# Performance work log

Measured on AMD Instinct MI355X. Metric: run time of the kernel, lower is better.

Reference implementation:

```python
import jax, jax.numpy as jnp
import numpy as np

WS = 7        # window_size
SHIFT = 3     # shift_size
HEADS = 6
DIM = 192
HIDDEN = DIM * 6  # mlp_ratio=6
EPS = 1e-5


def _rel_pos_index(ws):
    # static relative-position index, (ws*ws, ws*ws) int
    coords = np.stack(np.meshgrid(np.arange(ws), np.arange(ws), indexing='ij')).reshape(2, -1)
    rel = coords[:, :, None] - coords[:, None, :]            # (2, N, N)
    rel = rel.transpose(1, 2, 0)                             # (N, N, 2)
    rel[:, :, 0] += ws - 1
    rel[:, :, 1] += ws - 1
    rel[:, :, 0] *= 2 * ws - 1
    return rel.sum(-1)


def _layernorm(t, g, b):
    m = t.mean(-1, keepdims=True)
    v = jnp.mean((t - m) ** 2, axis=-1, keepdims=True)
    return (t - m) * jax.lax.rsqrt(v + EPS) * g + b


def setup_inputs() -> dict:
    key = jax.random.key(0)
    ks = jax.random.split(key, 8)
    B, H, W = 16, 56, 56
    x = jax.random.normal(ks[0], (B, H * W, DIM), dtype=jnp.float32)
    p = lambda k, s: (jax.random.normal(k, s, dtype=jnp.float32) * 0.02)
    return {
        'x': x, 'H': H, 'W': W,
        'ln1_g': jnp.ones((DIM,), jnp.float32), 'ln1_b': jnp.zeros((DIM,), jnp.float32),
        'qkv_w': p(ks[1], (3 * DIM, DIM)), 'qkv_b': jnp.zeros((3 * DIM,), jnp.float32),
        'rpb': p(ks[2], ((2 * WS - 1) ** 2, HEADS)),
        'proj_w': p(ks[3], (DIM, DIM)), 'proj_b': jnp.zeros((DIM,), jnp.float32),
        'ln2_g': jnp.ones((DIM,), jnp.float32), 'ln2_b': jnp.zeros((DIM,), jnp.float32),
        'fc1_w': p(ks[4], (HIDDEN, DIM)), 'fc1_b': jnp.zeros((HIDDEN,), jnp.float32),
        'fc2_w': p(ks[5], (DIM, HIDDEN)), 'fc2_b': jnp.zeros((DIM,), jnp.float32),
    }


def reference(x, H, W, ln1_g, ln1_b, qkv_w, qkv_b, rpb, proj_w, proj_b,
              ln2_g, ln2_b, fc1_w, fc1_b, fc2_w, fc2_b):
    B, L, C = x.shape
    hd = C // HEADS
    shortcut = x
    h = _layernorm(x, ln1_g, ln1_b).reshape(B, H, W, C)
    pad_r = (WS - W % WS) % WS
    pad_b = (WS - H % WS) % WS
    h = jnp.pad(h, ((0, 0), (0, pad_b), (0, pad_r), (0, 0)))
    Hp, Wp = H + pad_b, W + pad_r
    if SHIFT > 0:
        h = jnp.roll(h, (-SHIFT, -SHIFT), axis=(1, 2))
    # window partition -> (nW*B, WS*WS, C)
    h = h.reshape(B, Hp // WS, WS, Wp // WS, WS, C).transpose(0, 1, 3, 2, 4, 5)
    h = h.reshape(-1, WS * WS, C)
    nB, N, _ = h.shape
    qkv = (h @ qkv_w.T + qkv_b).reshape(nB, N, 3, HEADS, hd).transpose(2, 0, 3, 1, 4)
    q, k, v = qkv[0], qkv[1], qkv[2]       # (nB, heads, N, hd)
    scale = hd ** -0.5
    attn = jnp.einsum('bhnd,bhmd->bhnm', q * scale, k)
    idx = _rel_pos_index(WS)
    bias = rpb[idx.reshape(-1)].reshape(N, N, HEADS).transpose(2, 0, 1)  # (heads, N, N)
    attn = jax.nn.softmax(attn + bias[None], axis=-1)
    out = jnp.einsum('bhnm,bhmd->bhnd', attn, v).transpose(0, 2, 1, 3).reshape(nB, N, C)
    out = out @ proj_w.T + proj_b
    # window reverse -> (B, Hp, Wp, C)
    out = out.reshape(B, Hp // WS, Wp // WS, WS, WS, C).transpose(0, 1, 3, 2, 4, 5)
    out = out.reshape(B, Hp, Wp, C)
    if SHIFT > 0:
        out = jnp.roll(out, (SHIFT, SHIFT), axis=(1, 2))
    out = out[:, :H, :W, :].reshape(B, H * W, C)
    x = shortcut + out
    h2 = _layernorm(x, ln2_g, ln2_b)
    h2 = jax.nn.gelu(h2 @ fc1_w.T + fc1_b, approximate=False)
    return x + (h2 @ fc2_w.T + fc2_b)
```

## Files before the change

### kernel.cpp

```cpp
#include <hip/hip_runtime.h>

typedef unsigned short u16;
typedef __bf16 bf16x8 __attribute__((ext_vector_type(8)));
typedef __bf16 bf16x2_t __attribute__((ext_vector_type(2)));
typedef float f32x4 __attribute__((ext_vector_type(4)));

#define AS1 __attribute__((address_space(1)))
#define AS3 __attribute__((address_space(3)))

__device__ __forceinline__ void gld16(const void* g, void* l) {
  __builtin_amdgcn_global_load_lds((const AS1 void*)g, (AS3 void*)l, 16, 0, 0);
}

__device__ __forceinline__ u16 f2bf(float f) {
  union { float f; unsigned int u; } v; v.f = f;
  unsigned int u = v.u;
  u += 0x7fffu + ((u >> 16) & 1u);
  return (u16)(u >> 16);
}
__device__ __forceinline__ float bf2f(u16 h) {
  union { unsigned int u; float f; } v; v.u = ((unsigned int)h) << 16; return v.f;
}
__device__ __forceinline__ unsigned int pk2(float a, float b) {
#if __has_builtin(__builtin_amdgcn_cvt_pk_bf16_f32)
  union { bf16x2_t v; unsigned int u; } c;
  c.v = __builtin_amdgcn_cvt_pk_bf16_f32(a, b);
  return c.u;
#else
  return (unsigned int)f2bf(a) | ((unsigned int)f2bf(b) << 16);
#endif
}
__device__ __forceinline__ float gelu_f(float v) {
  float u = v * (1.5957691216f + 0.0713548163f * v * v);
  return v * __builtin_amdgcn_rcpf(1.0f + __expf(-u));
}

__global__ __launch_bounds__(256) void cast_weights(
    const float* __restrict__ w0, const float* __restrict__ w1,
    const float* __restrict__ w2, const float* __restrict__ w3,
    u16* __restrict__ o0, u16* __restrict__ o1,
    u16* __restrict__ o2, u16* __restrict__ o3) {
  int i = blockIdx.x * 256 + threadIdx.x;
  if (i < 110592) o0[i] = f2bf(w0[i]);
  if (i < 36864) {
    int n = i / 192, kp = i - n * 192;
    int h = kp >> 5, dp = kp & 31;
    int d = (dp & 1) ? ((dp >> 1) + 16) : (dp >> 1);
    o1[i] = f2bf(w1[n * 192 + h * 32 + d]);
  }
  if (i < 221184) o2[i] = f2bf(w2[i]);
  if (i < 221184) o3[i] = f2bf(w3[i]);
}

__global__ __launch_bounds__(256) void build_btab(
    const float* __restrict__ rpb, float* __restrict__ btab) {
  int id = blockIdx.x * 256 + threadIdx.x;
  int head = id >> 12;
  int m = (id >> 6) & 63;
  int r = id & 63;
  float v;
  if (m >= 49) v = -1e30f;
  else if (r >= 49) v = 0.0f;
  else {
    int mi = m / 7, mj = m - mi * 7;
    int ri = r / 7, rj = r - ri * 7;
    v = rpb[((ri - mi + 6) * 13 + (rj - mj + 6)) * 6 + head];
  }
  btab[id] = v;
}

__global__ __launch_bounds__(256) void ln_kernel(
    const float* __restrict__ x, const float* __restrict__ g,
    const float* __restrict__ b, u16* __restrict__ out) {
  int row = blockIdx.x * 4 + (threadIdx.x >> 6);
  int lane = threadIdx.x & 63;
  const float* xr = x + (long)row * 192;
  float e0 = xr[lane], e1 = xr[lane + 64], e2 = xr[lane + 128];
  float s = e0 + e1 + e2;
  #pragma unroll
  for (int o = 1; o < 64; o <<= 1) s += __shfl_xor(s, o);
  float mean = s * (1.0f / 192.0f);
  float d0 = e0 - mean, d1 = e1 - mean, d2 = e2 - mean;
  float q = d0 * d0 + d1 * d1 + d2 * d2;
  #pragma unroll
  for (int o = 1; o < 64; o <<= 1) q += __shfl_xor(q, o);
  float rstd = rsqrtf(q * (1.0f / 192.0f) + 1e-5f);
  u16* orow = out + (long)row * 192;
  orow[lane]       = f2bf(d0 * rstd * g[lane]       + b[lane]);
  orow[lane + 64]  = f2bf(d1 * rstd * g[lane + 64]  + b[lane + 64]);
  orow[lane + 128] = f2bf(d2 * rstd * g[lane + 128] + b[lane + 128]);
}

template<int MODE>
__global__ __launch_bounds__(256, 3) void wsgemm_kernel(
    const u16* __restrict__ A, const u16* __restrict__ W,
    const float* __restrict__ bias, const float* __restrict__ resid,
    void* __restrict__ out, int N) {
  __shared__ u16 wlds[36 * 512];
  const int tid = threadIdx.x;
  const int wave = tid >> 6, lane = tid & 63;
  const int quad = lane >> 4, l15 = lane & 15;
  const int bn = blockIdx.y * 96;
  const long bm = (long)blockIdx.x * 128 + wave * 32;

  bf16x8 af[2][6];
  #pragma unroll
  for (int mt = 0; mt < 2; mt++)
    #pragma unroll
    for (int kc = 0; kc < 6; kc++)
      af[mt][kc] = *(const bf16x8*)&A[(bm + mt * 16 + l15) * 192 + kc * 32 + quad * 8];

  #pragma unroll
  for (int i = 0; i < 9; i++) {
    int t = wave + i * 4;
    int kc = t / 6, nt = t - kc * 6;
    gld16(W + (long)(bn + nt * 16 + l15) * 192 + kc * 32 + quad * 8,
          &wlds[t * 512]);
  }

  float bi[6];
  #pragma unroll
  for (int nt = 0; nt < 6; nt++) bi[nt] = bias[bn + nt * 16 + l15];

  __syncthreads();

  f32x4 acc[2][6] = {};
  #pragma unroll
  for (int kc = 0; kc < 6; kc++) {
    #pragma unroll
    for (int nt = 0; nt < 6; nt++) {
      bf16x8 wf = *(const bf16x8*)&wlds[(kc * 6 + nt) * 512 + lane * 8];
      acc[0][nt] = __builtin_amdgcn_mfma_f32_16x16x32_bf16(af[0][kc], wf, acc[0][nt], 0, 0, 0);
      acc[1][nt] = __builtin_amdgcn_mfma_f32_16x16x32_bf16(af[1][kc], wf, acc[1][nt], 0, 0, 0);
    }
  }

  #pragma unroll
  for (int mt = 0; mt < 2; mt++) {
    #pragma unroll
    for (int nt = 0; nt < 6; nt++) {
      const long col = bn + nt * 16 + l15;
      #pragma unroll
      for (int j = 0; j < 4; j++) {
        const long row = bm + mt * 16 + quad * 4 + j;
        const long idx = row * (long)N + col;
        float v = acc[mt][nt][j] + bi[nt];
        if (MODE == 2) {
          ((float*)out)[idx] = v + resid[idx];
        } else {
          if (MODE == 1) v = gelu_f(v);
          ((u16*)out)[idx] = f2bf(v);
        }
      }
    }
  }
}

template<int MODE>
__global__ __launch_bounds__(256, 3) void gemm_kernel(
    const u16* __restrict__ A, const u16* __restrict__ W,
    const float* __restrict__ bias, const float* __restrict__ resid,
    void* __restrict__ out, int N, int K) {
  constexpr int TT = 20;
  constexpr int BUF = TT * 512;
  __shared__ u16 lds[2 * BUF];
  float* ct = (float*)lds;
  const int tid = threadIdx.x;
  const int wave = tid >> 6, lane = tid & 63;
  const int wm = wave >> 1, wn = wave & 1;
  const int quad = lane >> 4, l15 = lane & 15;
  const long bm = (long)blockIdx.x * 128;
  const int bn = blockIdx.y * 192;
  const int NC = K >> 5;

  const u16* sp[5];
  int sd[5];
  #pragma unroll
  for (int i = 0; i < 5; i++) {
    int t = wave + i * 4;
    sp[i] = (t < 8) ? (A + (bm + t * 16 + l15) * (long)K + quad * 8)
                    : (W + (long)(bn + (t - 8) * 16 + l15) * K + quad * 8);
    sd[i] = t * 512;
  }
  auto stage = [&](u16* dst) {
    #pragma unroll
    for (int i = 0; i < 5; i++) { gld16(sp[i], dst + sd[i]); sp[i] += 32; }
  };

  stage(lds);
  __syncthreads();

  f32x4 acc[4][6] = {};
  for (int c = 0; c < NC; c++) {
    const int cur = c & 1;
    if (c + 1 < NC) stage(&lds[(cur ^ 1) * BUF]);
    const u16* buf = lds + cur * BUF;
    bf16x8 af[4];
    #pragma unroll
    for (int mt = 0; mt < 4; mt++)
      af[mt] = *(const bf16x8*)&buf[(wm * 4 + mt) * 512 + lane * 8];
    #pragma unroll
    for (int nt = 0; nt < 6; nt++) {
      bf16x8 bfr = *(const bf16x8*)&buf[(8 + wn * 6 + nt) * 512 + lane * 8];
      #pragma unroll
      for (int mt = 0; mt < 4; mt++)
        acc[mt][nt] = __builtin_amdgcn_mfma_f32_16x16x32_bf16(af[mt], bfr, acc[mt][nt], 0, 0, 0);
    }
    __syncthreads();
  }

  const int frow = tid >> 2, seg = tid & 3;
  #pragma unroll
  for (int h = 0; h < 2; h++) {
    #pragma unroll
    for (int g = 0; g < 2; g++) {
      if (wm == h && wn == g) {
        #pragma unroll
        for (int nt = 0; nt < 6; nt++) {
          int col = nt * 16 + l15;
          float bi = bias[bn + g * 96 + col];
          #pragma unroll
          for (int mt = 0; mt < 4; mt++) {
            int row0 = mt * 16 + quad * 4;
            #pragma unroll
            for (int j = 0; j < 4; j++)
              ct[(row0 + j) * 100 + col] = acc[mt][nt][j] + bi;
          }
        }
      }
      __syncthreads();
      const float* cp = &ct[frow * 100 + seg * 4];
      long gbase = (bm + h * 64 + frow) * (long)N + bn + g * 96 + seg * 4;
      #pragma unroll
      for (int k = 0; k < 6; k++) {
        float4 v = *(const float4*)(cp + k * 16);
        long idx = gbase + k * 16;
        if (MODE == 2) {
          const float4 rv = *(const float4*)(resid + idx);
          v.x += rv.x; v.y += rv.y; v.z += rv.z; v.w += rv.w;
          *(float4*)((float*)out + idx) = v;
        } else {
          if (MODE == 1) {
            v.x = gelu_f(v.x); v.y = gelu_f(v.y); v.z = gelu_f(v.z); v.w = gelu_f(v.w);
          }
          uint2 pk;
          pk.x = pk2(v.x, v.y);
          pk.y = pk2(v.z, v.w);
          *(uint2*)((u16*)out + idx) = pk;
        }
      }
      if (!(h == 1 && g == 1)) __syncthreads();
    }
  }
}

__global__ __launch_bounds__(256) void attn_kernel(
    const u16* __restrict__ qkv, const float* __restrict__ btab,
    u16* __restrict__ attn) {
  __shared__ u16 lds[4 * 7040];
  __shared__ float sbias[64 * 65];
  int tid = threadIdx.x;
  int wave = tid >> 6, lane = tid & 63;
  int quad = lane >> 4, l15 = lane & 15;
  int head = blockIdx.x % 6;
  int grp = blockIdx.x / 6;
  int win = grp * 4 + wave;
  int b = win >> 6, wy = (win >> 3) & 7, wx = win & 7;
  u16* lp = lds + wave * 7040;
  u16* lvt = lp + 4608;
  float* rsum = (float*)(lp + 6912);

  {
    const float* bsrc = btab + head * 4096;
    #pragma unroll
    for (int i = 0; i < 4; i++) {
      int idx4 = tid + i * 256;
      float4 v = *(const float4*)(bsrc + idx4 * 4);
      float* dst = &sbias[(idx4 >> 4) * 65 + (idx4 & 15) * 4];
      dst[0] = v.x; dst[1] = v.y; dst[2] = v.z; dst[3] = v.w;
    }
  }

  bf16x8 qb[4], ka[4];
  #pragma unroll
  for (int t = 0; t < 4; t++) {
    int n = t * 16 + l15;
    uint4 qv = {0, 0, 0, 0}, kv = {0, 0, 0, 0}, vv = {0, 0, 0, 0};
    if (n < 49) {
      int i = n / 7, j = n - i * 7;
      int y = wy * 7 + i + 3;  if (y >= 56) y -= 56;
      int xx = wx * 7 + j + 3; if (xx >= 56) xx -= 56;
      long base = ((long)(b * 3136 + y * 56 + xx)) * 576 + head * 32 + quad * 8;
      qv = *(const uint4*)(qkv + base);
      kv = *(const uint4*)(qkv + base + 192);
      vv = *(const uint4*)(qkv + base + 384);
    }
    qb[t] = *(const bf16x8*)&qv;
    ka[t] = *(const bf16x8*)&kv;
    const u16* vp = (const u16*)&vv;
    #pragma unroll
    for (int d = 0; d < 8; d++) lvt[(quad * 8 + d) * 72 + n] = vp[d];
  }

  f32x4 s[4][4];
  const f32x4 fz = {0.0f, 0.0f, 0.0f, 0.0f};
  #pragma unroll
  for (int tm = 0; tm < 4; tm++)
    #pragma unroll
    for (int tr = 0; tr < 4; tr++)
      s[tm][tr] = __builtin_amdgcn_mfma_f32_16x16x32_bf16(ka[tm], qb[tr], fz, 0, 0, 0);

  __syncthreads();

  const float scale = 0.17677669529663687f;
  float mx[4] = {-1e30f, -1e30f, -1e30f, -1e30f};
  #pragma unroll
  for (int tm = 0; tm < 4; tm++) {
    int m0 = tm * 16 + quad * 4;
    #pragma unroll
    for (int tr = 0; tr < 4; tr++) {
      int r = tr * 16 + l15;
      #pragma unroll
      for (int j = 0; j < 4; j++) {
        float v = s[tm][tr][j] * scale + sbias[(m0 + j) * 65 + r];
        s[tm][tr][j] = v;
        mx[tr] = fmaxf(mx[tr], v);
      }
    }
  }
  #pragma unroll
  for (int tr = 0; tr < 4; tr++) {
    mx[tr] = fmaxf(mx[tr], __shfl_xor(mx[tr], 16));
    mx[tr] = fmaxf(mx[tr], __shfl_xor(mx[tr], 32));
  }
  float sm[4] = {0.f, 0.f, 0.f, 0.f};
  #pragma unroll
  for (int tm = 0; tm < 4; tm++) {
    #pragma unroll
    for (int tr = 0; tr < 4; tr++) {
      int r = tr * 16 + l15;
      float e0 = __expf(s[tm][tr][0] - mx[tr]);
      float e1 = __expf(s[tm][tr][1] - mx[tr]);
      float e2 = __expf(s[tm][tr][2] - mx[tr]);
      float e3 = __expf(s[tm][tr][3] - mx[tr]);
      sm[tr] += (e0 + e1) + (e2 + e3);
      uint2 pk;
      pk.x = pk2(e0, e1);
      pk.y = pk2(e2, e3);
      *(uint2*)&lp[r * 72 + tm * 16 + quad * 4] = pk;
    }
  }
  #pragma unroll
  for (int tr = 0; tr < 4; tr++) {
    sm[tr] += __shfl_xor(sm[tr], 16);
    sm[tr] += __shfl_xor(sm[tr], 32);
  }
  if (quad == 0) {
    #pragma unroll
    for (int tr = 0; tr < 4; tr++) rsum[tr * 16 + l15] = __builtin_amdgcn_rcpf(sm[tr]);
  }

  f32x4 o[4][2] = {};
  #pragma unroll
  for (int ks = 0; ks < 2; ks++) {
    bf16x8 vb0 = *(const bf16x8*)&lvt[(l15) * 72 + ks * 32 + quad * 8];
    bf16x8 vb1 = *(const bf16x8*)&lvt[(16 + l15) * 72 + ks * 32 + quad * 8];
    #pragma unroll
    for (int rt = 0; rt < 4; rt++) {
      bf16x8 pf = *(const bf16x8*)&lp[(rt * 16 + l15) * 72 + ks * 32 + quad * 8];
      o[rt][0] = __builtin_amdgcn_mfma_f32_16x16x32_bf16(pf, vb0, o[rt][0], 0, 0, 0);
      o[rt][1] = __builtin_amdgcn_mfma_f32_16x16x32_bf16(pf, vb1, o[rt][1], 0, 0, 0);
    }
  }
  #pragma unroll
  for (int rt = 0; rt < 4; rt++) {
    #pragma unroll
    for (int j = 0; j < 4; j++) {
      int r = rt * 16 + quad * 4 + j;
      if (r < 49) {
        float inv = rsum[r];
        int i = r / 7, jj = r - i * 7;
        int y = wy * 7 + i + 3;   if (y >= 56) y -= 56;
        int xx = wx * 7 + jj + 3; if (xx >= 56) xx -= 56;
        long base = ((long)(b * 3136 + y * 56 + xx)) * 192 + head * 32 + 2 * l15;
        *(unsigned int*)&attn[base] = pk2(o[rt][0][j] * inv, o[rt][1][j] * inv);
      }
    }
  }
}

extern "C" void kernel_launch(void* const* d_in, const int* in_sizes, int n_in,
                              void* d_out, int out_size, void* d_ws, size_t ws_size,
                              hipStream_t stream) {
  (void)in_sizes; (void)n_in; (void)out_size; (void)ws_size;
  const float* x      = (const float*)d_in[0];
  const float* ln1_g  = (const float*)d_in[3];
  const float* ln1_b  = (const float*)d_in[4];
  const float* qkv_w  = (const float*)d_in[5];
  const float* qkv_b  = (const float*)d_in[6];
  const float* rpb    = (const float*)d_in[7];
  const float* proj_w = (const float*)d_in[8];
  const float* proj_b = (const float*)d_in[9];
  const float* ln2_g  = (const float*)d_in[10];
  const float* ln2_b  = (const float*)d_in[11];
  const float* fc1_w  = (const float*)d_in[12];
  const float* fc1_b  = (const float*)d_in[13];
  const float* fc2_w  = (const float*)d_in[14];
  const float* fc2_b  = (const float*)d_in[15];

  char* ws = (char*)d_ws;
  float* x2   = (float*)(ws + 0);
  u16* hA     = (u16*)(ws + 38535168);
  float* btab = (float*)(ws + 38535168);
  u16* qkv    = (u16*)(ws + 57802752);
  u16* attn   = (u16*)(ws + 115605504);
  u16* hid    = (u16*)(ws + 57802752);
  u16* wbuf   = (u16*)(ws + 173408256);
  u16* qkv_wb  = wbuf;
  u16* proj_wb = wbuf + 110592;
  u16* fc1_wb  = wbuf + 147456;
  u16* fc2_wb  = wbuf + 368640;

  cast_weights<<<dim3(864), 256, 0, stream>>>(qkv_w, proj_w, fc1_w, fc2_w,
                                              qkv_wb, proj_wb, fc1_wb, fc2_wb);
  ln_kernel<<<dim3(12544), 256, 0, stream>>>(x, ln1_g, ln1_b, hA);
  wsgemm_kernel<0><<<dim3(392, 6), 256, 0, stream>>>(hA, qkv_wb, qkv_b, nullptr,
                                                     qkv, 576);
  build_btab<<<dim3(96), 256, 0, stream>>>(rpb, btab);
  attn_kernel<<<dim3(1536), 256, 0, stream>>>(qkv, btab, attn);
  wsgemm_kernel<2><<<dim3(392, 2), 256, 0, stream>>>(attn, proj_wb, proj_b, x,
                                                     x2, 192);
  ln_kernel<<<dim3(12544), 256, 0, stream>>>(x2, ln2_g, ln2_b, hA);
  wsgemm_kernel<1><<<dim3(392, 12), 256, 0, stream>>>(hA, fc1_wb, fc1_b, nullptr,
                                                      hid, 1152);
  gemm_kernel<2><<<dim3(392, 1), 256, 0, stream>>>(hid, fc2_wb, fc2_b, x2,
                                                   (float*)d_out, 192, 1152);
}
```

Measured before the change: 324.3 us.

## Replace fc2 GEMM with wave-split kernel loading A directly to registers

The fc2 GEMM (K=1152) switches from a double-buffered LDS kernel that stages both A and W to a new kernel. In it, each wave loads its own 32 rows of A straight from global memory into registers, and only the weight tile is staged in LDS, in 192-wide K chunks. The grid doubles to 392x2 with 96-column tiles for more parallelism, and the epilogue writes results directly instead of transposing through LDS. The trade-offs are uncoalesced scalar fp32 stores, A being read twice (once per column tile), and no overlap between loads and MFMA within a chunk.

```diff
diff --git a/kernel.cpp b/kernel.cpp
--- a/kernel.cpp
+++ b/kernel.cpp
@@ -156,100 +156,70 @@
   }
 }
 
-template<int MODE>
-__global__ __launch_bounds__(256, 3) void gemm_kernel(
+__global__ __launch_bounds__(256, 3) void wsgemm2_kernel(
     const u16* __restrict__ A, const u16* __restrict__ W,
     const float* __restrict__ bias, const float* __restrict__ resid,
-    void* __restrict__ out, int N, int K) {
-  constexpr int TT = 20;
-  constexpr int BUF = TT * 512;
-  __shared__ u16 lds[2 * BUF];
-  float* ct = (float*)lds;
+    float* __restrict__ out, int N) {
+  __shared__ u16 wlds[36 * 512];
   const int tid = threadIdx.x;
   const int wave = tid >> 6, lane = tid & 63;
-  const int wm = wave >> 1, wn = wave & 1;
   const int quad = lane >> 4, l15 = lane & 15;
-  const long bm = (long)blockIdx.x * 128;
-  const int bn = blockIdx.y * 192;
-  const int NC = K >> 5;
-
-  const u16* sp[5];
-  int sd[5];
-  #pragma unroll
-  for (int i = 0; i < 5; i++) {
+  const int bn = blockIdx.y * 96;
+  const long bm = (long)blockIdx.x * 128 + wave * 32;
+
+  const u16* pa0 = A + (bm + l15) * 1152 + quad * 8;
+  const u16* pa1 = pa0 + 16 * 1152;
+  const u16* wp[9];
+  int wd[9];
+  #pragma unroll
+  for (int i = 0; i < 9; i++) {
     int t = wave + i * 4;
-    sp[i] = (t < 8) ? (A + (bm + t * 16 + l15) * (long)K + quad * 8)
-                    : (W + (long)(bn + (t - 8) * 16 + l15) * K + quad * 8);
-    sd[i] = t * 512;
-  }
-  auto stage = [&](u16* dst) {
-    #pragma unroll
-    for (int i = 0; i < 5; i++) { gld16(sp[i], dst + sd[i]); sp[i] += 32; }
-  };
-
-  stage(lds);
-  __syncthreads();
-
-  f32x4 acc[4][6] = {};
-  for (int c = 0; c < NC; c++) {
-    const int cur = c & 1;
-    if (c + 1 < NC) stage(&lds[(cur ^ 1) * BUF]);
-    const u16* buf = lds + cur * BUF;
-    bf16x8 af[4];
-    #pragma unroll
-    for (int mt = 0; mt < 4; mt++)
-      af[mt] = *(const bf16x8*)&buf[(wm * 4 + mt) * 512 + lane * 8];
+    int kc = t / 6, nt = t - kc * 6;
+    wp[i] = W + (long)(bn + nt * 16 + l15) * 1152 + kc * 32 + quad * 8;
+    wd[i] = t * 512;
+  }
+
+  f32x4 acc[2][6] = {};
+  #pragma unroll
+  for (int c = 0; c < 6; c++) {
+    if (c) __syncthreads();
+    bf16x8 af0[6], af1[6];
+    #pragma unroll
+    for (int kc = 0; kc < 6; kc++) {
+      af0[kc] = *(const bf16x8*)(pa0 + kc * 32);
+      af1[kc] = *(const bf16x8*)(pa1 + kc * 32);
+    }
+    #pragma unroll
+    for (int i = 0; i < 9; i++) gld16(wp[i], &wlds[wd[i]]);
+    __syncthreads();
+    #pragma unroll
+    for (int kc = 0; kc < 6; kc++) {
+      #pragma unroll
+      for (int nt = 0; nt < 6; nt++) {
+        bf16x8 wf = *(const bf16x8*)&wlds[(kc * 6 + nt) * 512 + lane * 8];
+        acc[0][nt] = __builtin_amdgcn_mfma_f32_16x16x32_bf16(af0[kc], wf, acc[0][nt], 0, 0, 0);
+        acc[1][nt] = __builtin_amdgcn_mfma_f32_16x16x32_bf16(af1[kc], wf, acc[1][nt], 0, 0, 0);
+      }
+    }
+    pa0 += 192; pa1 += 192;
+    #pragma unroll
+    for (int i = 0; i < 9; i++) wp[i] += 192;
+  }
+
+  float bi[6];
+  #pragma unroll
+  for (int nt = 0; nt < 6; nt++) bi[nt] = bias[bn + nt * 16 + l15];
+  #pragma unroll
+  for (int mt = 0; mt < 2; mt++) {
     #pragma unroll
     for (int nt = 0; nt < 6; nt++) {
-      bf16x8 bfr = *(const bf16x8*)&buf[(8 + wn * 6 + nt) * 512 + lane * 8];
+      const long col = bn + nt * 16 + l15;
       #pragma unroll
-      for (int mt = 0; mt < 4; mt++)
-        acc[mt][nt] = __builtin_amdgcn_mfma_f32_16x16x32_bf16(af[mt], bfr, acc[mt][nt], 0, 0, 0);
-    }
-    __syncthreads();
-  }
-
-  const int frow = tid >> 2, seg = tid & 3;
-  #pragma unroll
-  for (int h = 0; h < 2; h++) {
-    #pragma unroll
-    for (int g = 0; g < 2; g++) {
-      if (wm == h && wn == g) {
-        #pragma unroll
-        for (int nt = 0; nt < 6; nt++) {
-          int col = nt * 16 + l15;
-          float bi = bias[bn + g * 96 + col];
-          #pragma unroll
-          for (int mt = 0; mt < 4; mt++) {
-            int row0 = mt * 16 + quad * 4;
-            #pragma unroll
-            for (int j = 0; j < 4; j++)
-              ct[(row0 + j) * 100 + col] = acc[mt][nt][j] + bi;
-          }
-        }
+      for (int j = 0; j < 4; j++) {
+        const long row = bm + mt * 16 + quad * 4 + j;
+        const long idx = row * (long)N + col;
+        out[idx] = acc[mt][nt][j] + bi[nt] + resid[idx];
       }
-      __syncthreads();
-      const float* cp = &ct[frow * 100 + seg * 4];
-      long gbase = (bm + h * 64 + frow) * (long)N + bn + g * 96 + seg * 4;
-      #pragma unroll
-      for (int k = 0; k < 6; k++) {
-        float4 v = *(const float4*)(cp + k * 16);
-        long idx = gbase + k * 16;
-        if (MODE == 2) {
-          const float4 rv = *(const float4*)(resid + idx);
-          v.x += rv.x; v.y += rv.y; v.z += rv.z; v.w += rv.w;
-          *(float4*)((float*)out + idx) = v;
-        } else {
-          if (MODE == 1) {
-            v.x = gelu_f(v.x); v.y = gelu_f(v.y); v.z = gelu_f(v.z); v.w = gelu_f(v.w);
-          }
-          uint2 pk;
-          pk.x = pk2(v.x, v.y);
-          pk.y = pk2(v.z, v.w);
-          *(uint2*)((u16*)out + idx) = pk;
-        }
-      }
-      if (!(h == 1 && g == 1)) __syncthreads();
     }
   }
 }
@@ -433,6 +403,6 @@
   ln_kernel<<<dim3(12544), 256, 0, stream>>>(x2, ln2_g, ln2_b, hA);
   wsgemm_kernel<1><<<dim3(392, 12), 256, 0, stream>>>(hA, fc1_wb, fc1_b, nullptr,
                                                       hid, 1152);
-  gemm_kernel<2><<<dim3(392, 1), 256, 0, stream>>>(hid, fc2_wb, fc2_b, x2,
-                                                   (float*)d_out, 192, 1152);
-}
+  wsgemm2_kernel<<<dim3(392, 2), 256, 0, stream>>>(hid, fc2_wb, fc2_b, x2,
+                                                   (float*)d_out, 192);
+}
```

New measurement: 359.4 us. 10.8% more time.
